# Kernel tuning notes

Hardware: AMD Instinct MI355X
Metric: run time of the kernel (lower is better)

Reference implementation:

```python
import jax, jax.numpy as jnp
import numpy as np

HEADS = 16
HEAD_DIM = 64
HIDDEN = HEADS * HEAD_DIM          # 1024
EXP = 4
QKVFF = HIDDEN * (3 + EXP)         # 7168
VFF = HIDDEN * (1 + EXP)           # 5120
B, L = 2, 2048
LN_EPS = 1e-5


def setup_inputs() -> dict:
    key = jax.random.key(0)
    k1, k2, k3 = jax.random.split(key, 3)
    x = jax.random.normal(k1, (B, L, HIDDEN), dtype=jnp.float32)
    W_in = jax.random.normal(k2, (HIDDEN, QKVFF), dtype=jnp.float32) * (HIDDEN ** -0.5)
    W_out = jax.random.normal(k3, (VFF, HIDDEN), dtype=jnp.float32) * (VFF ** -0.5)
    ln_w = jnp.ones((HIDDEN,), dtype=jnp.float32)
    ln_b = jnp.zeros((HIDDEN,), dtype=jnp.float32)
    return {"x": x, "ln_w": ln_w, "ln_b": ln_b, "W_in": W_in, "W_out": W_out}


def _rotary_tables(l, dtype):
    inv_freq = 1.0 / (10000.0 ** (jnp.arange(0, HEAD_DIM, 2, dtype=jnp.float32) / HEAD_DIM))
    t = jnp.arange(l, dtype=jnp.float32)
    freqs = t[:, None] * inv_freq[None, :]            # [l, d/2]
    emb = jnp.concatenate([freqs, freqs], axis=-1)     # [l, d]
    return jnp.cos(emb).astype(dtype), jnp.sin(emb).astype(dtype)


def _rotate_half(x):
    x1, x2 = jnp.split(x, 2, axis=-1)
    return jnp.concatenate([-x2, x1], axis=-1)


def reference(x, ln_w, ln_b, W_in, W_out):
    b, l, d = x.shape
    # shared LayerNorm
    mu = jnp.mean(x, axis=-1, keepdims=True)
    var = jnp.var(x, axis=-1, keepdims=True)
    xn = (x - mu) * jax.lax.rsqrt(var + LN_EPS) * ln_w + ln_b
    # fused in-projection
    h = xn @ W_in                                      # [b, l, qkvff]
    q, k, v, ff = jnp.split(h, [HIDDEN, 2 * HIDDEN, 3 * HIDDEN], axis=-1)
    q = q.reshape(b, l, HEADS, HEAD_DIM)
    k = k.reshape(b, l, HEADS, HEAD_DIM)
    v = v.reshape(b, l, HEADS, HEAD_DIM)
    # inline RoPE on q, k
    cos, sin = _rotary_tables(l, x.dtype)              # [l, d]
    cos = cos[None, :, None, :]
    sin = sin[None, :, None, :]
    q = q * cos + _rotate_half(q) * sin
    k = k * cos + _rotate_half(k) * sin
    # causal attention with explicit mask bias (as in the original)
    a = jnp.einsum('bihd,bjhd->bhij', q, k) * (HEAD_DIM ** -0.5)
    causal = jnp.tril(jnp.ones((l, l), dtype=a.dtype))
    a = a + (-1e10) * (1.0 - causal)
    a = jax.nn.softmax(a, axis=-1)
    o = jnp.einsum('bhij,bjhd->bihd', a, v).reshape(b, l, HIDDEN)
    # parallel FF branch
    ff = jax.nn.gelu(ff, approximate=False)
    return jnp.concatenate([o, ff], axis=-1) @ W_out
```

## Files before the change

kernel.cpp:

```cpp
#include <hip/hip_runtime.h>
#include <math.h>

#define HEADS 16
#define HEAD_DIM 64
#define HIDDEN 1024
#define NQKVFF 7168
#define VFF 5120
#define SEQ 2048
#define MROWS 4096

typedef unsigned short u16;
typedef __attribute__((ext_vector_type(8))) short bf16x8;
typedef __attribute__((ext_vector_type(4))) float f32x4;
typedef __attribute__((address_space(1))) void gas_void;
typedef __attribute__((address_space(3))) void las_void;

__device__ inline u16 f2bf(float f) {
    union { float f; unsigned u; } v; v.f = f;
    unsigned r = v.u + 0x7FFFu + ((v.u >> 16) & 1u);
    return (u16)(r >> 16);
}
__device__ inline float bf2f(u16 h) {
    union { unsigned u; float f; } v; v.u = ((unsigned)h) << 16;
    return v.f;
}

__global__ __launch_bounds__(256) void ln_kernel(const float* __restrict__ x,
        const float* __restrict__ w, const float* __restrict__ b,
        u16* __restrict__ xn) {
    int row = blockIdx.x;
    int tid = threadIdx.x;
    const float* xr = x + (size_t)row * HIDDEN;
    float4 v = ((const float4*)xr)[tid];
    float s = v.x + v.y + v.z + v.w;
    float sq = v.x * v.x + v.y * v.y + v.z * v.z + v.w * v.w;
    for (int off = 32; off > 0; off >>= 1) {
        s += __shfl_down(s, off, 64);
        sq += __shfl_down(sq, off, 64);
    }
    __shared__ float ls[4], lsq[4];
    int wid = tid >> 6, lane = tid & 63;
    if (lane == 0) { ls[wid] = s; lsq[wid] = sq; }
    __syncthreads();
    float ts = ls[0] + ls[1] + ls[2] + ls[3];
    float tsq = lsq[0] + lsq[1] + lsq[2] + lsq[3];
    float mu = ts * (1.0f / HIDDEN);
    float var = tsq * (1.0f / HIDDEN) - mu * mu;
    float rstd = rsqrtf(var + 1e-5f);
    float4 wv = ((const float4*)w)[tid];
    float4 bv = ((const float4*)b)[tid];
    ushort4 o;
    o.x = f2bf((v.x - mu) * rstd * wv.x + bv.x);
    o.y = f2bf((v.y - mu) * rstd * wv.y + bv.y);
    o.z = f2bf((v.z - mu) * rstd * wv.z + bv.z);
    o.w = f2bf((v.w - mu) * rstd * wv.w + bv.w);
    ((ushort4*)(xn + (size_t)row * HIDDEN))[tid] = o;
}

__global__ __launch_bounds__(256) void transpose_f2b(const float* __restrict__ in,
        u16* __restrict__ out, int R, int C) {
    __shared__ u16 tile[32][33];
    int c0 = blockIdx.x * 32, r0 = blockIdx.y * 32;
    int tx = threadIdx.x & 31, ty = threadIdx.x >> 5;
#pragma unroll
    for (int k = 0; k < 4; k++)
        tile[ty + k * 8][tx] = f2bf(in[(size_t)(r0 + ty + k * 8) * C + c0 + tx]);
    __syncthreads();
#pragma unroll
    for (int k = 0; k < 4; k++)
        out[(size_t)(c0 + ty + k * 8) * R + r0 + tx] = tile[tx][ty + k * 8];
}

__device__ inline void gemm_core_128(const u16* __restrict__ A, int lda,
                                     const u16* __restrict__ BT, int ldb,
                                     int Klen, int bm, int bn, f32x4 acc[4][4],
                                     u16* lds) {
    const int tid = threadIdx.x;
    const int wid = tid >> 6;
    const int lane = tid & 63;
    const int quad = lane >> 4;
    const int cc = lane & 15;
    const int wm = (wid >> 1) * 64;
    const int wn = (wid & 1) * 64;
#pragma unroll
    for (int i = 0; i < 4; i++)
#pragma unroll
        for (int j = 0; j < 4; j++)
#pragma unroll
            for (int r = 0; r < 4; r++) acc[i][j][r] = 0.0f;

    const int row = tid >> 2;
    const int gch = ((tid & 3) ^ ((row >> 1) & 3)) * 8;
    const int slot = (quad ^ ((cc >> 1) & 3)) * 8;
    const int lofs = (tid & 192) * 8;

    u16* cur = lds;
    u16* nxt = lds + 8192;

#pragma unroll
    for (int I = 0; I < 2; I++) {
        int r128 = I * 64 + row;
        const u16* ga = A + (size_t)(bm + r128) * lda + gch;
        __builtin_amdgcn_global_load_lds((gas_void*)ga,
                (las_void*)(cur + I * 2048 + lofs), 16, 0, 0);
        const u16* gb = BT + (size_t)(bn + r128) * ldb + gch;
        __builtin_amdgcn_global_load_lds((gas_void*)gb,
                (las_void*)(cur + 4096 + I * 2048 + lofs), 16, 0, 0);
    }
    __syncthreads();

    for (int k0 = 0; k0 < Klen; k0 += 32) {
        const bool more = (k0 + 32 < Klen);
        if (more) {
#pragma unroll
            for (int I = 0; I < 2; I++) {
                int r128 = I * 64 + row;
                const u16* ga = A + (size_t)(bm + r128) * lda + k0 + 32 + gch;
                __builtin_amdgcn_global_load_lds((gas_void*)ga,
                        (las_void*)(nxt + I * 2048 + lofs), 16, 0, 0);
                const u16* gb = BT + (size_t)(bn + r128) * ldb + k0 + 32 + gch;
                __builtin_amdgcn_global_load_lds((gas_void*)gb,
                        (las_void*)(nxt + 4096 + I * 2048 + lofs), 16, 0, 0);
            }
        }
        bf16x8 af[4], bfr[4];
#pragma unroll
        for (int t = 0; t < 4; t++) {
            af[t]  = *(const bf16x8*)(cur + (wm + t * 16 + cc) * 32 + slot);
            bfr[t] = *(const bf16x8*)(cur + 4096 + (wn + t * 16 + cc) * 32 + slot);
        }
        __builtin_amdgcn_s_setprio(1);
#pragma unroll
        for (int i = 0; i < 4; i++)
#pragma unroll
            for (int j = 0; j < 4; j++)
                acc[i][j] = __builtin_amdgcn_mfma_f32_16x16x32_bf16(af[i], bfr[j], acc[i][j], 0, 0, 0);
        __builtin_amdgcn_s_setprio(0);
        if (more) __syncthreads();
        u16* tmp = cur; cur = nxt; nxt = tmp;
    }
}

__device__ inline float gelu_f(float v) {
    float u = v * (v * v * 0.044715f + 1.0f) * 0.7978845608028654f;
    u = fminf(u, 15.0f);
    float e = exp2f(u * 2.8853900817779268f);
    return v * (e / (e + 1.0f));
}

__global__ __launch_bounds__(256) void gemm1(const u16* __restrict__ xn,
        const u16* __restrict__ WinT, u16* __restrict__ qkb,
        u16* __restrict__ vtb, u16* __restrict__ a2) {
    __shared__ u16 lds[2 * 8192];
    int bm = blockIdx.x * 128, bn = blockIdx.y * 128;
    f32x4 acc[4][4];
    gemm_core_128(xn, HIDDEN, WinT, HIDDEN, HIDDEN, bm, bn, acc, lds);
    const int tid = threadIdx.x, wid = tid >> 6, lane = tid & 63;
    const int quad = lane >> 4, cc = lane & 15;
    const int wm = (wid >> 1) * 64, wn = (wid & 1) * 64;
    const int m0 = bm + wm;
    const int b = m0 >> 11;

    if (bn >= 3072) {
#pragma unroll
        for (int i = 0; i < 4; i++)
#pragma unroll
            for (int j = 0; j < 4; j++)
#pragma unroll
                for (int r = 0; r < 4; r++) {
                    int m = m0 + i * 16 + quad * 4 + r;
                    int n = bn + wn + j * 16 + cc;
                    a2[(size_t)m * VFF + (n - 2048)] = f2bf(gelu_f(acc[i][j][r]));
                }
    } else if (bn >= 2048) {
        int hh = ((bn - 2048 + wn) >> 6) & 15;
        u16* dst = vtb + (size_t)(b * 16 + hh) * (HEAD_DIM * SEQ);
#pragma unroll
        for (int i = 0; i < 4; i++) {
            int key0 = (m0 + i * 16 + quad * 4) & 2047;
            size_t ob = (size_t)(key0 >> 5) * 2048 +
                        (((key0 & 31) >> 3) * 16 + cc) * 8 + (key0 & 7);
#pragma unroll
            for (int jf = 0; jf < 4; jf++) {
                ushort4 o;
                o.x = f2bf(acc[i][jf][0]);
                o.y = f2bf(acc[i][jf][1]);
                o.z = f2bf(acc[i][jf][2]);
                o.w = f2bf(acc[i][jf][3]);
                *(ushort4*)(dst + ob + jf * 512) = o;
            }
        }
    } else {
        int t = bn >> 10;
        int hh = ((bn + wn) >> 6) & 15;
        u16* base = qkb + (size_t)(t * 32 + b * 16 + hh) * (SEQ * HEAD_DIM);
        float scale = t ? 1.0f : 0.18033688011112043f;
        float f0 = expf(cc * -0.28782313662425572f);
        float f1 = expf((16 + cc) * -0.28782313662425572f);
        const int o0 = ((cc >> 3) * 16) * 8 + (cc & 7);
        const int o1 = ((2 + (cc >> 3)) * 16) * 8 + (cc & 7);
#pragma unroll
        for (int i = 0; i < 4; i++)
#pragma unroll
            for (int r = 0; r < 4; r++) {
                int pos = (m0 + i * 16 + quad * 4 + r) & 2047;
                int ob = (pos >> 4) * 1024 + (pos & 15) * 8;
                float s_, c_;
                __sincosf(pos * f0, &s_, &c_);
                float x1 = acc[i][0][r], x2 = acc[i][2][r];
                base[ob + o0]       = f2bf((x1 * c_ - x2 * s_) * scale);
                base[ob + o0 + 512] = f2bf((x2 * c_ + x1 * s_) * scale);
                __sincosf(pos * f1, &s_, &c_);
                x1 = acc[i][1][r]; x2 = acc[i][3][r];
                base[ob + o1]       = f2bf((x1 * c_ - x2 * s_) * scale);
                base[ob + o1 + 512] = f2bf((x2 * c_ + x1 * s_) * scale);
            }
    }
}

__global__ __launch_bounds__(256) void gemm2(const u16* __restrict__ a2,
        const u16* __restrict__ WoutT, float* __restrict__ p0, float* __restrict__ p1) {
    __shared__ u16 lds[2 * 8192];
    int bm = blockIdx.x * 128, bn = blockIdx.y * 128;
    int split = blockIdx.z;
    float* dst = split ? p1 : p0;
    f32x4 acc[4][4];
    gemm_core_128(a2 + split * 2560, VFF, WoutT + split * 2560, VFF, 2560,
                  bm, bn, acc, lds);
    const int tid = threadIdx.x, wid = tid >> 6, lane = tid & 63;
    const int quad = lane >> 4, cc = lane & 15;
    const int wm = (wid >> 1) * 64, wn = (wid & 1) * 64;
#pragma unroll
    for (int i = 0; i < 4; i++)
#pragma unroll
        for (int j = 0; j < 4; j++)
#pragma unroll
            for (int r = 0; r < 4; r++) {
                int m = bm + wm + i * 16 + quad * 4 + r;
                int n = bn + wn + j * 16 + cc;
                dst[(size_t)m * HIDDEN + n] = acc[i][j][r];
            }
}

__global__ __launch_bounds__(256) void reduce2(const float* __restrict__ p0,
        const float* __restrict__ p1, float* __restrict__ out) {
    int i = blockIdx.x * 256 + threadIdx.x;
    float4 a = ((const float4*)p0)[i];
    float4 b = ((const float4*)p1)[i];
    a.x += b.x; a.y += b.y; a.z += b.z; a.w += b.w;
    ((float4*)out)[i] = a;
}

__global__ __launch_bounds__(256) void attn_kernel(const u16* __restrict__ qk,
        const u16* __restrict__ vt, u16* __restrict__ a2) {
    const int id  = blockIdx.x;
    const int bh  = (id & 7) * 4 + ((id >> 3) & 3);
    const int bx  = id >> 5;
    const int tid = threadIdx.x;
    const int wid = tid >> 6;
    const int lane = tid & 63;
    const int quad = lane >> 4;
    const int cc = lane & 15;
    const int slot = wid >> 1;
    const int parity = wid & 1;
    const int tile = slot ? (127 - bx) : bx;
    const int q0 = tile * 16;

    const u16* Qp = qk + (size_t)bh * (SEQ * HEAD_DIM);
    const u16* Kp = qk + (size_t)(32 + bh) * (SEQ * HEAD_DIM);
    const u16* VP = vt + (size_t)bh * (HEAD_DIM * SEQ);

    __shared__ u16 Pbuf[4][16 * 72];
    __shared__ float obuf[2][64 * 17];
    __shared__ float lbuf[2][16];
    u16* P = Pbuf[wid];

    const int bb = bh >> 4, hh = bh & 15;
    const int qcol = q0 + cc;

    bf16x8 qa0 = *(const bf16x8*)(Qp + (q0 >> 4) * 1024 + lane * 8);
    bf16x8 qa1 = *(const bf16x8*)(Qp + (q0 >> 4) * 1024 + 512 + lane * 8);

    float ps = 0.0f;
    f32x4 ot[4];
#pragma unroll
    for (int mt = 0; mt < 4; mt++)
#pragma unroll
        for (int r = 0; r < 4; r++) ot[mt][r] = 0.0f;

    for (int kb = parity * 64; kb < q0 + 16; kb += 128) {
        const bool diag = (kb + 64 > q0);
        f32x4 s[4];
        __builtin_amdgcn_s_setprio(1);
#pragma unroll
        for (int c = 0; c < 4; c++) {
            s[c][0] = -32.0f; s[c][1] = -32.0f; s[c][2] = -32.0f; s[c][3] = -32.0f;
            const u16* kblob = Kp + ((kb >> 4) + c) * 1024 + lane * 8;
            bf16x8 ka0 = *(const bf16x8*)(kblob);
            bf16x8 ka1 = *(const bf16x8*)(kblob + 512);
            s[c] = __builtin_amdgcn_mfma_f32_16x16x32_bf16(ka0, qa0, s[c], 0, 0, 0);
            s[c] = __builtin_amdgcn_mfma_f32_16x16x32_bf16(ka1, qa1, s[c], 0, 0, 0);
        }
        __builtin_amdgcn_s_setprio(0);
        bf16x8 vf[2][4];
#pragma unroll
        for (int kc = 0; kc < 2; kc++)
#pragma unroll
            for (int mt = 0; mt < 4; mt++)
                vf[kc][mt] = *(const bf16x8*)(VP + ((kb >> 5) + kc) * 2048 + mt * 512 + lane * 8);
        if (diag) {
#pragma unroll
            for (int c = 0; c < 4; c++)
#pragma unroll
                for (int r = 0; r < 4; r++) {
                    int key = kb + c * 16 + quad * 4 + r;
                    s[c][r] = (key <= qcol) ? s[c][r] : -10000.0f;
                }
        }
#pragma unroll
        for (int c = 0; c < 4; c++) {
            float p0v = exp2f(s[c][0]); ps += p0v;
            float p1v = exp2f(s[c][1]); ps += p1v;
            float p2v = exp2f(s[c][2]); ps += p2v;
            float p3v = exp2f(s[c][3]); ps += p3v;
            unsigned r0, r1;
            asm("v_cvt_pk_bf16_f32 %0, %1, %2" : "=v"(r0) : "v"(p0v), "v"(p1v));
            asm("v_cvt_pk_bf16_f32 %0, %1, %2" : "=v"(r1) : "v"(p2v), "v"(p3v));
            uint2 pk; pk.x = r0; pk.y = r1;
            *(uint2*)(P + cc * 72 + c * 16 + quad * 4) = pk;
        }
        asm volatile("s_waitcnt lgkmcnt(0)" ::: "memory");
        __builtin_amdgcn_s_setprio(1);
#pragma unroll
        for (int kc = 0; kc < 2; kc++) {
            bf16x8 pb = *(const bf16x8*)(P + cc * 72 + kc * 32 + quad * 8);
#pragma unroll
            for (int mt = 0; mt < 4; mt++)
                ot[mt] = __builtin_amdgcn_mfma_f32_16x16x32_bf16(vf[kc][mt], pb, ot[mt], 0, 0, 0);
        }
        __builtin_amdgcn_s_setprio(0);
    }

    ps += __shfl_xor(ps, 16, 64);
    ps += __shfl_xor(ps, 32, 64);

    if (parity == 1) {
        if (quad == 0) lbuf[slot][cc] = ps;
        float* ob = obuf[slot] + lane * 17;
#pragma unroll
        for (int mt = 0; mt < 4; mt++)
#pragma unroll
            for (int r = 0; r < 4; r++) ob[mt * 4 + r] = ot[mt][r];
    }
    __syncthreads();
    if (parity == 0) {
        float l = ps + lbuf[slot][cc];
        float rl = 1.0f / l;
        const float* ob = obuf[slot] + lane * 17;
        u16* dst = a2 + ((size_t)(bb * SEQ + q0 + cc)) * VFF + hh * 64;
#pragma unroll
        for (int mt = 0; mt < 4; mt++) {
            ushort4 o;
            o.x = f2bf((ot[mt][0] + ob[mt * 4 + 0]) * rl);
            o.y = f2bf((ot[mt][1] + ob[mt * 4 + 1]) * rl);
            o.z = f2bf((ot[mt][2] + ob[mt * 4 + 2]) * rl);
            o.w = f2bf((ot[mt][3] + ob[mt * 4 + 3]) * rl);
            *(ushort4*)(dst + mt * 16 + quad * 4) = o;
        }
    }
}

extern "C" void kernel_launch(void* const* d_in, const int* in_sizes, int n_in,
                              void* d_out, int out_size, void* d_ws, size_t ws_size,
                              hipStream_t stream) {
    const float* x     = (const float*)d_in[0];
    const float* ln_w  = (const float*)d_in[1];
    const float* ln_b  = (const float*)d_in[2];
    const float* W_in  = (const float*)d_in[3];
    const float* W_out = (const float*)d_in[4];
    float* out = (float*)d_out;
    char* ws = (char*)d_ws;
    u16* xn    = (u16*)(ws);
    u16* WinT  = (u16*)(ws + 8388608);
    u16* qkb   = (u16*)(ws + 23068672);
    u16* vtb   = (u16*)(ws + 39845888);
    u16* WoutT = (u16*)(ws + 48234496);
    u16* a2    = (u16*)(ws + 58720256);
    float* p0  = (float*)(ws);
    float* p1  = (float*)(ws + 16777216);

    ln_kernel<<<dim3(MROWS), dim3(256), 0, stream>>>(x, ln_w, ln_b, xn);
    transpose_f2b<<<dim3(NQKVFF / 32, HIDDEN / 32), dim3(256), 0, stream>>>(W_in, WinT, HIDDEN, NQKVFF);
    transpose_f2b<<<dim3(HIDDEN / 32, VFF / 32), dim3(256), 0, stream>>>(W_out, WoutT, VFF, HIDDEN);
    gemm1<<<dim3(MROWS / 128, NQKVFF / 128), dim3(256), 0, stream>>>(xn, WinT, qkb, vtb, a2);
    attn_kernel<<<dim3(2048), dim3(256), 0, stream>>>(qkb, vtb, a2);
    gemm2<<<dim3(MROWS / 128, HIDDEN / 128, 2), dim3(256), 0, stream>>>(a2, WoutT, p0, p1);
    reduce2<<<dim3(MROWS * HIDDEN / 4 / 256), dim3(256), 0, stream>>>(p0, p1, out);
}
```

Measured before the change: 306.2 us.

## Enlarge gemm1 tile to 256x256 with 512 threads and double-buffered swizzled LDS

Rewrites the in-projection GEMM to use 256x256 output tiles computed by 8 waves, each wave owning a 128x64 sub-tile, with K-step 64 staged via direct global-to-LDS loads into an XOR-swizzled double buffer. The goal is higher arithmetic intensity and fewer global loads per MFMA than the 128x128 tiles, and fewer bank conflicts on LDS reads. The cost is 128KB of LDS and many accumulator registers per thread, which limits occupancy. The grid also drops to 16x28 blocks, which may underfill the GPU's CUs.

Result: faster. 290.1 us (-5.3%).

```diff
diff --git a/kernel.cpp b/kernel.cpp
--- a/kernel.cpp
+++ b/kernel.cpp
@@ -8,6 +8,7 @@
 #define VFF 5120
 #define SEQ 2048
 #define MROWS 4096
+#define G1NT 16
 
 typedef unsigned short u16;
 typedef __attribute__((ext_vector_type(8))) short bf16x8;
@@ -141,6 +142,18 @@
     }
 }
 
+__device__ __forceinline__ void stage_half_256(const u16* __restrict__ src,
+        int ld, int row0, int k0, u16* dsthalf, int tid) {
+#pragma unroll
+    for (int I = 0; I < 2; I++) {
+        int r = (tid >> 3) + I * 64;
+        int g = (tid & 7) ^ ((r >> 1) & 7);
+        const u16* ga = src + (size_t)(row0 + r) * ld + k0 + g * 8;
+        __builtin_amdgcn_global_load_lds((gas_void*)ga,
+                (las_void*)(dsthalf + I * 4096 + (tid & 0x1C0) * 8), 16, 0, 0);
+    }
+}
+
 __device__ inline float gelu_f(float v) {
     float u = v * (v * v * 0.044715f + 1.0f) * 0.7978845608028654f;
     u = fminf(u, 15.0f);
@@ -148,35 +161,102 @@
     return v * (e / (e + 1.0f));
 }
 
-__global__ __launch_bounds__(256) void gemm1(const u16* __restrict__ xn,
+__global__ __launch_bounds__(512, 2) void gemm1(const u16* __restrict__ xn,
         const u16* __restrict__ WinT, u16* __restrict__ qkb,
         u16* __restrict__ vtb, u16* __restrict__ a2) {
-    __shared__ u16 lds[2 * 8192];
-    int bm = blockIdx.x * 128, bn = blockIdx.y * 128;
-    f32x4 acc[4][4];
-    gemm_core_128(xn, HIDDEN, WinT, HIDDEN, HIDDEN, bm, bn, acc, lds);
-    const int tid = threadIdx.x, wid = tid >> 6, lane = tid & 63;
-    const int quad = lane >> 4, cc = lane & 15;
-    const int wm = (wid >> 1) * 64, wn = (wid & 1) * 64;
-    const int m0 = bm + wm;
+    __shared__ u16 lds[2 * 32768];
+    const int tid = threadIdx.x;
+    const int wid = tid >> 6;
+    const int lane = tid & 63;
+    const int quad = lane >> 4;
+    const int cc = lane & 15;
+    const int wr = wid >> 2;
+    const int wc = wid & 3;
+    const int bm = blockIdx.x * 256, bn = blockIdx.y * 256;
+    const int wrbase = wr * 128;
+    const int wcbase = wc * 64;
+
+    f32x4 acc[8][4];
+#pragma unroll
+    for (int i = 0; i < 8; i++)
+#pragma unroll
+        for (int j = 0; j < 4; j++)
+#pragma unroll
+            for (int r = 0; r < 4; r++) acc[i][j][r] = 0.0f;
+
+    stage_half_256(xn,   HIDDEN, bm,       0, lds,                 tid);
+    stage_half_256(xn,   HIDDEN, bm + 128, 0, lds + 8192,          tid);
+    stage_half_256(WinT, HIDDEN, bn,       0, lds + 16384,         tid);
+    stage_half_256(WinT, HIDDEN, bn + 128, 0, lds + 16384 + 8192,  tid);
+
+#pragma unroll 1
+    for (int t = 0; t < G1NT; ++t) {
+        asm volatile("s_waitcnt vmcnt(0)\n\ts_barrier" ::: "memory");
+        const u16* buf = lds + (t & 1) * 32768;
+        if (t + 1 < G1NT) {
+            u16* nbuf = lds + ((t + 1) & 1) * 32768;
+            int k1 = (t + 1) * 64;
+            stage_half_256(xn,   HIDDEN, bm,       k1, nbuf,                tid);
+            stage_half_256(xn,   HIDDEN, bm + 128, k1, nbuf + 8192,         tid);
+            stage_half_256(WinT, HIDDEN, bn,       k1, nbuf + 16384,        tid);
+            stage_half_256(WinT, HIDDEN, bn + 128, k1, nbuf + 16384 + 8192, tid);
+        }
+#pragma unroll
+        for (int mh = 0; mh < 2; mh++) {
+            bf16x8 af[4][2];
+#pragma unroll
+            for (int i2 = 0; i2 < 4; i2++) {
+                int r = wrbase + (mh * 4 + i2) * 16 + cc;
+                const u16* pa = buf + ((r >> 7) << 13) + ((r & 127) << 6);
+                int sw = (r >> 1) & 7;
+                af[i2][0] = *(const bf16x8*)(pa + ((quad ^ sw) << 3));
+                af[i2][1] = *(const bf16x8*)(pa + (((4 + quad) ^ sw) << 3));
+            }
+#pragma unroll
+            for (int nh = 0; nh < 2; nh++) {
+                bf16x8 bfr[2][2];
+#pragma unroll
+                for (int j2 = 0; j2 < 2; j2++) {
+                    int r = wcbase + (nh * 2 + j2) * 16 + cc;
+                    const u16* pb = buf + 16384 + ((r >> 7) << 13) + ((r & 127) << 6);
+                    int sw = (r >> 1) & 7;
+                    bfr[j2][0] = *(const bf16x8*)(pb + ((quad ^ sw) << 3));
+                    bfr[j2][1] = *(const bf16x8*)(pb + (((4 + quad) ^ sw) << 3));
+                }
+                __builtin_amdgcn_s_setprio(1);
+#pragma unroll
+                for (int i2 = 0; i2 < 4; i2++)
+#pragma unroll
+                    for (int j2 = 0; j2 < 2; j2++) {
+                        int ii = mh * 4 + i2, jj = nh * 2 + j2;
+                        acc[ii][jj] = __builtin_amdgcn_mfma_f32_16x16x32_bf16(af[i2][0], bfr[j2][0], acc[ii][jj], 0, 0, 0);
+                        acc[ii][jj] = __builtin_amdgcn_mfma_f32_16x16x32_bf16(af[i2][1], bfr[j2][1], acc[ii][jj], 0, 0, 0);
+                    }
+                __builtin_amdgcn_s_setprio(0);
+            }
+        }
+    }
+
+    const int m0 = bm + wrbase;
     const int b = m0 >> 11;
-
-    if (bn >= 3072) {
-#pragma unroll
-        for (int i = 0; i < 4; i++)
+    const int nb = bn + wcbase;
+
+    if (nb >= 3072) {
+#pragma unroll
+        for (int i = 0; i < 8; i++)
 #pragma unroll
             for (int j = 0; j < 4; j++)
 #pragma unroll
                 for (int r = 0; r < 4; r++) {
                     int m = m0 + i * 16 + quad * 4 + r;
-                    int n = bn + wn + j * 16 + cc;
+                    int n = nb + j * 16 + cc;
                     a2[(size_t)m * VFF + (n - 2048)] = f2bf(gelu_f(acc[i][j][r]));
                 }
-    } else if (bn >= 2048) {
-        int hh = ((bn - 2048 + wn) >> 6) & 15;
+    } else if (nb >= 2048) {
+        int hh = ((nb - 2048) >> 6) & 15;
         u16* dst = vtb + (size_t)(b * 16 + hh) * (HEAD_DIM * SEQ);
 #pragma unroll
-        for (int i = 0; i < 4; i++) {
+        for (int i = 0; i < 8; i++) {
             int key0 = (m0 + i * 16 + quad * 4) & 2047;
             size_t ob = (size_t)(key0 >> 5) * 2048 +
                         (((key0 & 31) >> 3) * 16 + cc) * 8 + (key0 & 7);
@@ -191,16 +271,16 @@
             }
         }
     } else {
-        int t = bn >> 10;
-        int hh = ((bn + wn) >> 6) & 15;
-        u16* base = qkb + (size_t)(t * 32 + b * 16 + hh) * (SEQ * HEAD_DIM);
-        float scale = t ? 1.0f : 0.18033688011112043f;
+        int tq = nb >> 10;
+        int hh = (nb >> 6) & 15;
+        u16* base = qkb + (size_t)(tq * 32 + b * 16 + hh) * (SEQ * HEAD_DIM);
+        float scale = tq ? 1.0f : 0.18033688011112043f;
         float f0 = expf(cc * -0.28782313662425572f);
         float f1 = expf((16 + cc) * -0.28782313662425572f);
         const int o0 = ((cc >> 3) * 16) * 8 + (cc & 7);
         const int o1 = ((2 + (cc >> 3)) * 16) * 8 + (cc & 7);
 #pragma unroll
-        for (int i = 0; i < 4; i++)
+        for (int i = 0; i < 8; i++)
 #pragma unroll
             for (int r = 0; r < 4; r++) {
                 int pos = (m0 + i * 16 + quad * 4 + r) & 2047;
@@ -392,7 +472,7 @@
     ln_kernel<<<dim3(MROWS), dim3(256), 0, stream>>>(x, ln_w, ln_b, xn);
     transpose_f2b<<<dim3(NQKVFF / 32, HIDDEN / 32), dim3(256), 0, stream>>>(W_in, WinT, HIDDEN, NQKVFF);
     transpose_f2b<<<dim3(HIDDEN / 32, VFF / 32), dim3(256), 0, stream>>>(W_out, WoutT, VFF, HIDDEN);
-    gemm1<<<dim3(MROWS / 128, NQKVFF / 128), dim3(256), 0, stream>>>(xn, WinT, qkb, vtb, a2);
+    gemm1<<<dim3(MROWS / 256, NQKVFF / 256), dim3(512), 0, stream>>>(xn, WinT, qkb, vtb, a2);
     attn_kernel<<<dim3(2048), dim3(256), 0, stream>>>(qkb, vtb, a2);
     gemm2<<<dim3(MROWS / 128, HIDDEN / 128, 2), dim3(256), 0, stream>>>(a2, WoutT, p0, p1);
     reduce2<<<dim3(MROWS * HIDDEN / 4 / 256), dim3(256), 0, stream>>>(p0, p1, out);
```
